# Optimization experiments

Measured on AMD Instinct MI355X. Metric: run time of the kernel, lower is better.

Reference implementation:

```python
import jax, jax.numpy as jnp
import numpy as np

L, N, D, R = 1024, 16384, 512, 128
PENALTY = -10000.0


def setup_inputs() -> dict:
    key = jax.random.key(0)
    k1, k2, k3, k4, k5 = jax.random.split(key, 5)
    unary_logits = jax.random.normal(k1, (L, N), jnp.float32)
    H = jax.random.normal(k2, (N, D), jnp.float32)
    limit = float(np.sqrt(6.0 / (D + D)))  # xavier_uniform for square W
    W = jax.random.uniform(k3, (D, D), jnp.float32, -limit, limit)
    gold = jax.random.randint(k4, (L,), 0, N)
    # dense reachability matrix: allowed[cur_label, prev_label]
    allowed = jax.random.bernoulli(k5, 0.05, (N, N))
    return {"unary_logits": unary_logits, "H": H, "W": W, "gold": gold,
            "allowed": allowed, "top_r": R}


def reference(unary_logits, H, W, gold, allowed, top_r):
    # --- candidate pruning: top_r distinct labels per step, sorted ---
    _, idx = jax.lax.top_k(unary_logits, top_r)      # [L, R]
    cand = jnp.sort(idx, axis=-1)                     # matches sorted(set(topi))

    # --- forward (alpha) recurrence over candidate sets ---
    alpha0 = jax.nn.log_softmax(jnp.take(unary_logits[0], cand[0]))

    def step(alpha, xs):
        prev, cur, u = xs                             # [R], [R], [N]
        pair = (H[prev] @ W) @ H[cur].T               # [R, R] bilinear
        mask = allowed[cur][:, prev].T                # mask[i, j] = prev_i reachable to cur_j
        pair = pair + jnp.where(mask, 0.0, PENALTY)
        new_alpha = (jax.scipy.special.logsumexp(alpha[:, None] + pair, axis=0)
                     + jax.nn.log_softmax(u[cur]))
        return new_alpha, None

    alpha_last, _ = jax.lax.scan(step, alpha0,
                                 (cand[:-1], cand[1:], unary_logits[1:]))
    logZ = jax.scipy.special.logsumexp(alpha_last)

    # --- gold path score ---
    t = jnp.arange(unary_logits.shape[0])
    score_unary = unary_logits[t, gold].sum()
    gp, gc = gold[:-1], gold[1:]
    trans = jnp.einsum('ld,de,le->l', H[gp], W, H[gc])
    score_pair = jnp.where(allowed[gc, gp], trans, PENALTY).sum()

    return logZ - (score_unary + score_pair)
```

## Files before the change

kernel.cpp:

```cpp
#include <hip/hip_runtime.h>

typedef unsigned short u16;
typedef __attribute__((ext_vector_type(8))) short s8v;
typedef __attribute__((ext_vector_type(8))) __bf16 bfv8;
typedef __attribute__((ext_vector_type(4))) float f32x4;

#define L_DIM 1024
#define N_DIM 16384
#define R_DIM 128
#define PEN  -10000.0f
#define MC_MIN 1e-35f

__device__ __forceinline__ float b2f(u16 x) { return __uint_as_float(((unsigned)x) << 16); }
__device__ __forceinline__ u16 f2bf(float f) {
    unsigned u = __float_as_uint(f);
    unsigned r = (u + 0x7FFFu + ((u >> 16) & 1u)) >> 16;
    return (u16)r;
}
__device__ __forceinline__ unsigned fmapu(float f) {
    unsigned u = __float_as_uint(f);
    return (u & 0x80000000u) ? ~u : (u | 0x80000000u);
}
__device__ __forceinline__ float funmap(unsigned u) {
    unsigned b = (u & 0x80000000u) ? (u & 0x7fffffffu) : ~u;
    return __uint_as_float(b);
}
__device__ __forceinline__ int mask_ok(const void* al, int fl, size_t idx) {
    if (fl) return ((const unsigned char*)al)[idx] != 0;
    return ((const unsigned*)al)[idx] != 0u;
}

__device__ __forceinline__ float blk_max(float x, float* scr) {
#pragma unroll
    for (int o = 32; o > 0; o >>= 1) x = fmaxf(x, __shfl_xor(x, o));
    __syncthreads();
    if ((threadIdx.x & 63) == 0) scr[threadIdx.x >> 6] = x;
    __syncthreads();
    return fmaxf(fmaxf(scr[0], scr[1]), fmaxf(scr[2], scr[3]));
}
__device__ __forceinline__ float blk_sum(float x, float* scr) {
#pragma unroll
    for (int o = 32; o > 0; o >>= 1) x += __shfl_xor(x, o);
    __syncthreads();
    if ((threadIdx.x & 63) == 0) scr[threadIdx.x >> 6] = x;
    __syncthreads();
    return scr[0] + scr[1] + scr[2] + scr[3];
}

__global__ void detect_k(const unsigned* __restrict__ a, int* __restrict__ flag) {
    int bad = 0;
    for (int i = threadIdx.x; i < 4096; i += 256) {
        unsigned w = a[i];
        if (w != 0u && w != 1u && w != 0x3F800000u) bad = 1;
    }
    if (bad) *flag = 1;
}

__global__ __launch_bounds__(256) void pack_mask_k(const void* __restrict__ al,
                                                   const int* __restrict__ flag,
                                                   unsigned* __restrict__ bits) {
    const size_t wi = (size_t)blockIdx.x * 256 + threadIdx.x;
    const int fl = *flag;
    unsigned out = 0u;
    if (fl) {
        const uint4* p = (const uint4*)((const unsigned char*)al + wi * 32);
        uint4 a = p[0], b = p[1];
        unsigned v[8] = {a.x, a.y, a.z, a.w, b.x, b.y, b.z, b.w};
#pragma unroll
        for (int q = 0; q < 8; ++q)
#pragma unroll
            for (int e = 0; e < 4; ++e)
                if ((v[q] >> (e * 8)) & 0xFFu) out |= 1u << (q * 4 + e);
    } else {
        const uint4* p = (const uint4*)((const unsigned*)al + wi * 32);
#pragma unroll
        for (int q = 0; q < 8; ++q) {
            uint4 a = p[q];
            if (a.x) out |= 1u << (q * 4 + 0);
            if (a.y) out |= 1u << (q * 4 + 1);
            if (a.z) out |= 1u << (q * 4 + 2);
            if (a.w) out |= 1u << (q * 4 + 3);
        }
    }
    bits[wi] = out;
}

__global__ __launch_bounds__(256) void topk_lsm_k(const float* __restrict__ U,
                                                  int* __restrict__ candg,
                                                  float* __restrict__ lsmg) {
    const int t = blockIdx.x;
    const float* row = U + (size_t)t * N_DIM;
    __shared__ unsigned hist[256];
    __shared__ int sel[2];
    __shared__ int cnts[2];
    __shared__ float vals[128];
    __shared__ int inds[128];
    __shared__ float scr[4];
    const int tid = threadIdx.x;
    unsigned prefix = 0;
    int kneed = 128;
    for (int pass = 0; pass < 4; ++pass) {
        const int sh = 24 - pass * 8;
        hist[tid] = 0;
        __syncthreads();
        for (int i = tid; i < N_DIM; i += 256) {
            unsigned u = __float_as_uint(row[i]);
            unsigned k = (u & 0x80000000u) ? ~u : (u | 0x80000000u);
            bool match = (pass == 0) || ((k >> (sh + 8)) == prefix);
            if (match) atomicAdd(&hist[(k >> sh) & 255u], 1u);
        }
        __syncthreads();
        if (tid == 0) {
            int acc = 0, d = 0;
            for (int dig = 255; dig >= 0; --dig) {
                int c = (int)hist[dig];
                if (acc + c >= kneed) { d = dig; break; }
                acc += c;
            }
            sel[0] = d; sel[1] = acc;
        }
        __syncthreads();
        kneed -= sel[1];
        prefix = (prefix << 8) | (unsigned)sel[0];
        __syncthreads();
    }
    const unsigned K = prefix;
    if (tid < 2) cnts[tid] = 0;
    if (tid < 128) { vals[tid] = -1.0e30f; inds[tid] = 0; }
    __syncthreads();
    for (int i = tid; i < N_DIM; i += 256) {
        float f = row[i];
        unsigned u = __float_as_uint(f);
        unsigned k = (u & 0x80000000u) ? ~u : (u | 0x80000000u);
        if (k > K) { int p = atomicAdd(&cnts[0], 1); if (p < 128) { vals[p] = f; inds[p] = i; } }
    }
    __syncthreads();
    const int cgt = min(cnts[0], 128);
    for (int i = tid; i < N_DIM; i += 256) {
        float f = row[i];
        unsigned u = __float_as_uint(f);
        unsigned k = (u & 0x80000000u) ? ~u : (u | 0x80000000u);
        if (k == K) {
            int p = atomicAdd(&cnts[1], 1);
            if (cgt + p < 128) { vals[cgt + p] = f; inds[cgt + p] = i; }
        }
    }
    __syncthreads();
    float xv = (tid < 128) ? vals[tid] : -3.0e38f;
    float mx = blk_max(xv, scr);
    float ex = (tid < 128) ? __expf(vals[tid] - mx) : 0.f;
    float sm = blk_sum(ex, scr);
    float lse = mx + __logf(fmaxf(sm, 1e-37f));
    if (tid < 128) {
        candg[t * 128 + tid] = min(max(inds[tid], 0), N_DIM - 1);
        lsmg[t * 128 + tid] = vals[tid] - lse;
    }
}

__global__ void cast_h_k(const float* __restrict__ H, u16* __restrict__ Hbf) {
    size_t base = ((size_t)blockIdx.x * 256 + threadIdx.x) * 4;
    float4 f = *(const float4*)(H + base);
    ushort4 o;
    o.x = f2bf(f.x); o.y = f2bf(f.y); o.z = f2bf(f.z); o.w = f2bf(f.w);
    *(ushort4*)(Hbf + base) = o;
}

__global__ __launch_bounds__(256) void gemm_hw_k(const float* __restrict__ H,
                                                 const float* __restrict__ W,
                                                 u16* __restrict__ HWbf) {
    const int r0 = blockIdx.x * 8;
    __shared__ float Hl[8][512];
    for (int idx = threadIdx.x; idx < 8 * 512; idx += 256) {
        int r = idx >> 9, k = idx & 511;
        Hl[r][k] = H[(size_t)(r0 + r) * 512 + k];
    }
    __syncthreads();
    const int c = threadIdx.x;
    float acc0[8], acc1[8];
#pragma unroll
    for (int r = 0; r < 8; ++r) { acc0[r] = 0.f; acc1[r] = 0.f; }
    for (int k = 0; k < 512; ++k) {
        float w0 = W[(size_t)k * 512 + c];
        float w1 = W[(size_t)k * 512 + c + 256];
#pragma unroll
        for (int r = 0; r < 8; ++r) {
            float h = Hl[r][k];
            acc0[r] += h * w0;
            acc1[r] += h * w1;
        }
    }
#pragma unroll
    for (int r = 0; r < 8; ++r) {
        HWbf[(size_t)(r0 + r) * 512 + c] = f2bf(acc0[r]);
        HWbf[(size_t)(r0 + r) * 512 + c + 256] = f2bf(acc1[r]);
    }
}

__global__ __launch_bounds__(256) void pair_k(const int* __restrict__ candg,
                                              const float* __restrict__ lsmg,
                                              const u16* __restrict__ HWbf,
                                              const u16* __restrict__ Hbf,
                                              const unsigned* __restrict__ bits,
                                              u16* __restrict__ Eg,
                                              float* __restrict__ cvec,
                                              float* __restrict__ gvec0) {
    const int t = blockIdx.x + 1;
    __shared__ __align__(16) u16 tile[2][128 * 64];
    __shared__ int sprev[128], scur[128];
    __shared__ unsigned maskw[128][4];
    __shared__ unsigned scm_u[128];
    __shared__ float cmf[128], cvf[128], wvv[128], scr[4];
    const int tid = threadIdx.x;
    if (tid < 128) {
        sprev[tid] = min(max(candg[(t - 1) * 128 + tid], 0), N_DIM - 1);
        scur[tid]  = min(max(candg[t * 128 + tid], 0), N_DIM - 1);
        scm_u[tid] = 0u;
    }
    __syncthreads();

    const int lane = tid & 63, w = tid >> 6;
    const int wr = w >> 1, wc = w & 1;
    const int srow = lane >> 3, slot = lane & 7;
    const int lq = lane & 15, lh = lane >> 4;

    const u16* pA[4]; const u16* pB[4]; int wadr[4];
#pragma unroll
    for (int q = 0; q < 4; ++q) {
        int r = (w * 4 + q) * 8 + srow;
        pA[q] = HWbf + (size_t)sprev[r] * 512 + slot * 8;
        pB[q] = Hbf  + (size_t)scur[r] * 512 + slot * 8;
        wadr[q] = r * 64 + ((slot ^ srow) * 8);
    }
    s8v rA[4], rB[4];
#pragma unroll
    for (int q = 0; q < 4; ++q) { rA[q] = *(const s8v*)pA[q]; rB[q] = *(const s8v*)pB[q]; }

    {
        const int j = tid & 127, ihalf = tid >> 7;
        const unsigned* rowp = bits + (size_t)scur[j] * 512;
        unsigned mw0 = 0u, mw1 = 0u;
#pragma unroll 8
        for (int kb = 0; kb < 32; ++kb) {
            int p0 = sprev[ihalf * 64 + kb];
            int p1 = sprev[ihalf * 64 + 32 + kb];
            mw0 |= ((rowp[p0 >> 5] >> (p0 & 31)) & 1u) << kb;
            mw1 |= ((rowp[p1 >> 5] >> (p1 & 31)) & 1u) << kb;
        }
        maskw[j][ihalf * 2]     = mw0;
        maskw[j][ihalf * 2 + 1] = mw1;
    }

    f32x4 acc[4][4];
#pragma unroll
    for (int a = 0; a < 4; ++a)
#pragma unroll
        for (int b = 0; b < 4; ++b) acc[a][b] = (f32x4){0.f, 0.f, 0.f, 0.f};

    for (int s = 0; s < 8; ++s) {
        __syncthreads();
#pragma unroll
        for (int q = 0; q < 4; ++q) {
            *(s8v*)&tile[0][wadr[q]] = rA[q];
            *(s8v*)&tile[1][wadr[q]] = rB[q];
        }
        __syncthreads();
        if (s < 7) {
#pragma unroll
            for (int q = 0; q < 4; ++q) {
                pA[q] += 64; pB[q] += 64;
                rA[q] = *(const s8v*)pA[q];
                rB[q] = *(const s8v*)pB[q];
            }
        }
#pragma unroll
        for (int kk = 0; kk < 2; ++kk) {
            bfv8 aF[4], bF[4];
            const int sl = (((kk << 2) | lh) ^ (lq & 7)) * 8;
#pragma unroll
            for (int b = 0; b < 4; ++b) {
                aF[b] = *(const bfv8*)&tile[0][(wr * 64 + b * 16 + lq) * 64 + sl];
                bF[b] = *(const bfv8*)&tile[1][(wc * 64 + b * 16 + lq) * 64 + sl];
            }
#pragma unroll
            for (int bi = 0; bi < 4; ++bi)
#pragma unroll
                for (int bj = 0; bj < 4; ++bj)
                    acc[bi][bj] = __builtin_amdgcn_mfma_f32_16x16x32_bf16(
                        aF[bi], bF[bj], acc[bi][bj], 0, 0, 0);
        }
    }

#pragma unroll
    for (int bj = 0; bj < 4; ++bj) {
        const int j = wc * 64 + bj * 16 + lq;
        float cm = -3.0e38f;
#pragma unroll
        for (int bi = 0; bi < 4; ++bi) {
#pragma unroll
            for (int r = 0; r < 4; ++r) {
                int i = wr * 64 + bi * 16 + lh * 4 + r;
                float v = acc[bi][bj][r];
                if (!((maskw[j][i >> 5] >> (i & 31)) & 1u)) v += PEN;
                acc[bi][bj][r] = v;
                cm = fmaxf(cm, v);
            }
        }
        cm = fmaxf(cm, __shfl_xor(cm, 16));
        cm = fmaxf(cm, __shfl_xor(cm, 32));
        if (lane < 16) atomicMax(&scm_u[j], fmapu(cm));
    }
    __syncthreads();
    if (tid < 128) {
        float cm = funmap(scm_u[tid]);
        cmf[tid] = cm;
        float cv = cm + lsmg[(size_t)t * 128 + tid];
        cvf[tid] = cv;
        cvec[(size_t)(t - 1) * 128 + tid] = cv;
    }
    __syncthreads();
    const int m = t - 1;
    const int roleA = ((m & 1) == 0) && (m != 1022);
    float xg = (tid < 128) ? cvf[tid] : -3.0e38f;
    float g = blk_max(xg, scr);
    if (tid == 0) gvec0[m] = g;
    if (tid < 128) wvv[tid] = roleA ? __expf(cvf[tid] - g) : 1.0f;
    __syncthreads();
    u16* Ebuf = &tile[0][0];
#pragma unroll
    for (int bj = 0; bj < 4; ++bj) {
        const int j = wc * 64 + bj * 16 + lq;
        const float cm = cmf[j];
        const float wj = wvv[j];
#pragma unroll
        for (int bi = 0; bi < 4; ++bi) {
#pragma unroll
            for (int r = 0; r < 4; ++r) {
                int i = wr * 64 + bi * 16 + lh * 4 + r;
                float e = __expf(acc[bi][bj][r] - cm);
                e = fminf(fmaxf(e, 0.f), 1.0f) * wj;
                Ebuf[i * 128 + j] = f2bf(e);
            }
        }
    }
    __syncthreads();
    u16* Eo = Eg + (size_t)(t - 1) * 16384;
    for (int idx = tid; idx < 2048; idx += 256)
        ((s8v*)Eo)[idx] = ((const s8v*)Ebuf)[idx];
}

__global__ __launch_bounds__(256) void score_k(const float* __restrict__ U,
                                               const int* __restrict__ gold,
                                               const void* __restrict__ allowed,
                                               const int* __restrict__ flag,
                                               const u16* __restrict__ HWbf,
                                               const u16* __restrict__ Hbf,
                                               float* __restrict__ accums) {
    const int t = blockIdx.x;
    __shared__ float scr[4];
    float part = 0.f;
    int gp = 0, gc = 0;
    if (t < L_DIM - 1) {
        gp = min(max(gold[t], 0), N_DIM - 1);
        gc = min(max(gold[t + 1], 0), N_DIM - 1);
        const u16* ar = HWbf + (size_t)gp * 512;
        const u16* br = Hbf + (size_t)gc * 512;
        for (int k = threadIdx.x; k < 512; k += 256)
            part += b2f(ar[k]) * b2f(br[k]);
    }
    float tot = blk_sum(part, scr);
    if (threadIdx.x == 0) {
        if (t < L_DIM - 1) {
            int ok = mask_ok(allowed, *flag, (size_t)gc * N_DIM + (size_t)gp);
            atomicAdd(&accums[1], ok ? tot : PEN);
        }
        int g0 = min(max(gold[t], 0), N_DIM - 1);
        atomicAdd(&accums[0], U[(size_t)t * N_DIM + g0]);
    }
}

__global__ __launch_bounds__(256) void mcomb_k(const u16* __restrict__ Gin,
                                               const float* __restrict__ cin,
                                               const float* __restrict__ gin,
                                               u16* __restrict__ Gout,
                                               float* __restrict__ cout,
                                               float* __restrict__ gout,
                                               int n_in, int last) {
    const int o = blockIdx.x;
    const int tid = threadIdx.x;
    __shared__ __align__(16) u16 As[128 * 136];
    __shared__ __align__(16) u16 BT[128 * 136];
    __shared__ float cb[128], rmc[128], wvv[128], scr[4];
    __shared__ unsigned scm[128];
    const u16* GA = Gin + (size_t)(2 * o) * 16384;
    u16* GO = Gout + (size_t)o * 16384;
    const int roleA = (!last) && ((o & 1) == 0);

    if (2 * o + 1 >= n_in) {
        if (tid < 128) {
            float cv = cin[(size_t)(2 * o) * 128 + tid];
            cb[tid] = cv;
            cout[(size_t)o * 128 + tid] = cv;
        }
        __syncthreads();
        float xg = (tid < 128) ? cb[tid] : -3.0e38f;
        float gp = blk_max(xg, scr);
        if (tid == 0 && gout) gout[o] = gp;
        if (tid < 128) {
            float d = cb[tid] - gp;
            wvv[tid] = roleA ? ((d > -80.f) ? __expf(d) : 0.f) : 1.0f;
        }
        __syncthreads();
        for (int idx = tid; idx < 2048; idx += 256) {
            s8v vv = ((const s8v*)GA)[idx];
            if (roleA) {
                const int j0 = (idx & 15) * 8;
#pragma unroll
                for (int e = 0; e < 8; ++e)
                    vv[e] = (short)f2bf(b2f((u16)vv[e]) * wvv[j0 + e]);
            }
            ((s8v*)GO)[idx] = vv;
        }
        return;
    }

    const float gA = gin[2 * o];
    const u16* GB = Gin + (size_t)(2 * o + 1) * 16384;
    if (tid < 128) {
        cb[tid] = cin[(size_t)(2 * o + 1) * 128 + tid];
        scm[tid] = 0u;
    }
    __syncthreads();
    if (tid < 128) {
        const s8v* src = (const s8v*)(GB + (size_t)tid * 128);
#pragma unroll
        for (int q = 0; q < 16; ++q) {
            s8v v = src[q];
#pragma unroll
            for (int e = 0; e < 8; ++e)
                BT[(q * 8 + e) * 136 + tid] = (u16)v[e];
        }
    } else {
        const int t0 = tid - 128;
#pragma unroll
        for (int q = 0; q < 16; ++q) {
            int gc = q * 128 + t0;
            int r = gc >> 4, qc = gc & 15;
            *(s8v*)&As[r * 136 + qc * 8] = *(const s8v*)(GA + (size_t)r * 128 + qc * 8);
        }
    }
    __syncthreads();

    const int lane = tid & 63, w = tid >> 6;
    const int wr = w >> 1, wc = w & 1;
    const int lq = lane & 15, lh = lane >> 4;
    f32x4 acc[4][4];
#pragma unroll
    for (int a = 0; a < 4; ++a)
#pragma unroll
        for (int b = 0; b < 4; ++b) acc[a][b] = (f32x4){0.f, 0.f, 0.f, 0.f};
#pragma unroll
    for (int kc = 0; kc < 4; ++kc) {
        bfv8 aF[4], bF[4];
        const int off = kc * 32 + lh * 8;
#pragma unroll
        for (int b = 0; b < 4; ++b) {
            aF[b] = *(const bfv8*)&As[(wr * 64 + b * 16 + lq) * 136 + off];
            bF[b] = *(const bfv8*)&BT[(wc * 64 + b * 16 + lq) * 136 + off];
        }
#pragma unroll
        for (int bi = 0; bi < 4; ++bi)
#pragma unroll
            for (int bj = 0; bj < 4; ++bj)
                acc[bi][bj] = __builtin_amdgcn_mfma_f32_16x16x32_bf16(
                    aF[bi], bF[bj], acc[bi][bj], 0, 0, 0);
    }
#pragma unroll
    for (int bj = 0; bj < 4; ++bj) {
        float cm = 0.f;
#pragma unroll
        for (int bi = 0; bi < 4; ++bi)
#pragma unroll
            for (int r = 0; r < 4; ++r) cm = fmaxf(cm, acc[bi][bj][r]);
        cm = fmaxf(cm, __shfl_xor(cm, 16));
        cm = fmaxf(cm, __shfl_xor(cm, 32));
        if (lane < 16) atomicMax(&scm[wc * 64 + bj * 16 + lq], __float_as_uint(cm));
    }
    __syncthreads();
    float cpv = -3.0e38f;
    if (tid < 128) {
        float mc = __uint_as_float(scm[tid]);
        if (mc > MC_MIN) {
            rmc[tid] = 1.0f / mc;
            cpv = cb[tid] + gA + __logf(mc);
            if (!(cpv > -1.0e29f)) cpv = -1.0e30f;
        } else {
            rmc[tid] = 0.f;
            cpv = -1.0e30f;
        }
        cout[(size_t)o * 128 + tid] = cpv;
    }
    float gp = blk_max(cpv, scr);
    if (tid == 0 && gout) gout[o] = gp;
    if (tid < 128) {
        float d = cpv - gp;
        wvv[tid] = roleA ? ((d > -80.f) ? __expf(d) : 0.f) : 1.0f;
    }
    __syncthreads();
#pragma unroll
    for (int bj = 0; bj < 4; ++bj) {
        const int k = wc * 64 + bj * 16 + lq;
        const float sc = rmc[k] * wvv[k];
#pragma unroll
        for (int bi = 0; bi < 4; ++bi)
#pragma unroll
            for (int r = 0; r < 4; ++r) {
                const int i = wr * 64 + bi * 16 + lh * 4 + r;
                float e = acc[bi][bj][r] * sc;
                e = fminf(fmaxf(e, 0.f), 1.0f);
                As[i * 136 + k] = f2bf(e);
            }
    }
    __syncthreads();
    for (int idx = tid; idx < 2048; idx += 256) {
        int r = idx >> 4, qc = idx & 15;
        *(s8v*)(GO + (size_t)r * 128 + qc * 8) = *(const s8v*)&As[r * 136 + qc * 8];
    }
}

__global__ __launch_bounds__(256) void tfinal2_k(const u16* __restrict__ G5,
                                                 const float* __restrict__ c5,
                                                 const float* __restrict__ lsmg,
                                                 const float* __restrict__ accums,
                                                 float* __restrict__ out) {
    __shared__ float v[128], ev[128], scr[4];
    __shared__ float psum[2][128];
    __shared__ __align__(16) u16 Gs[16384];
    const int tid = threadIdx.x;
    const int k = tid & 127, h = tid >> 7;
    if (tid < 128) v[tid] = lsmg[tid];
    __syncthreads();
    for (int s = 0; s < 32; ++s) {
        const u16* G = G5 + (size_t)s * 16384;
        for (int idx = tid; idx < 2048; idx += 256)
            ((s8v*)Gs)[idx] = ((const s8v*)G)[idx];
        float x = (tid < 128) ? v[tid] : -3.0e38f;
        float mv = blk_max(x, scr);
        if (tid < 128) {
            float d = v[tid] - mv;
            ev[tid] = (d > -80.f) ? __expf(d) : 0.f;
        }
        __syncthreads();
        float dot = 0.f;
        const int i0 = h * 64;
#pragma unroll 8
        for (int i = 0; i < 64; ++i)
            dot += ev[i0 + i] * b2f(Gs[(i0 + i) * 128 + k]);
        psum[h][k] = dot;
        __syncthreads();
        if (tid < 128) {
            float d = psum[0][tid] + psum[1][tid];
            v[tid] = (d > 0.f) ? (c5[s * 128 + tid] + mv + __logf(d)) : -1.0e30f;
        }
        __syncthreads();
    }
    float x = (tid < 128) ? v[tid] : -3.0e38f;
    float mz = blk_max(x, scr);
    float e = (tid < 128) ? __expf(v[tid] - mz) : 0.f;
    float sm = blk_sum(e, scr);
    if (tid == 0) out[0] = mz + __logf(fmaxf(sm, 1e-37f)) - (accums[0] + accums[1]);
}

extern "C" void kernel_launch(void* const* d_in, const int* in_sizes, int n_in,
                              void* d_out, int out_size, void* d_ws, size_t ws_size,
                              hipStream_t stream) {
    const float* U = (const float*)d_in[0];
    const float* H = (const float*)d_in[1];
    const float* W = (const float*)d_in[2];
    const int* gold = (const int*)d_in[3];
    const void* allowed = (const void*)d_in[4];

    char* ws = (char*)d_ws;
    float* accums = (float*)ws;
    int* flag = (int*)(ws + 8);
    size_t off = 256;
    int* cand = (int*)(ws + off);     off += (size_t)L_DIM * R_DIM * 4;
    float* lsm = (float*)(ws + off);  off += (size_t)L_DIM * R_DIM * 4;
    u16* Hbf = (u16*)(ws + off);      off += (size_t)N_DIM * 512 * 2;
    u16* HWbf = (u16*)(ws + off);     off += (size_t)N_DIM * 512 * 2;
    u16* E = (u16*)(ws + off);        off += (size_t)(L_DIM - 1) * 16384 * 2;
    float* cvec = (float*)(ws + off); off += (size_t)(L_DIM - 1) * 128 * 4;
    unsigned* bitsw = (unsigned*)(ws + off); off += (size_t)N_DIM * (N_DIM / 8);
    float* gvec0 = (float*)(ws + off); off += 1024 * 4;
    float* c1 = (float*)(ws + off); off += 512 * 128 * 4;
    float* g1 = (float*)(ws + off); off += 512 * 4;
    float* c2 = (float*)(ws + off); off += 256 * 128 * 4;
    float* g2 = (float*)(ws + off); off += 256 * 4;
    float* c3 = (float*)(ws + off); off += 128 * 128 * 4;
    float* g3 = (float*)(ws + off); off += 128 * 4;
    float* c4 = (float*)(ws + off); off += 64 * 128 * 4;
    float* g4 = (float*)(ws + off); off += 64 * 4;
    float* c5 = (float*)(ws + off); off += 32 * 128 * 4;

    u16* G1 = Hbf;
    u16* G2 = HWbf;
    u16* G3 = Hbf;
    u16* G4 = HWbf;
    u16* G5 = Hbf;

    hipMemsetAsync(d_ws, 0, 256, stream);
    detect_k<<<1, 256, 0, stream>>>((const unsigned*)d_in[4], flag);
    pack_mask_k<<<(int)(((size_t)N_DIM * N_DIM / 32) / 256), 256, 0, stream>>>(allowed, flag, bitsw);
    topk_lsm_k<<<L_DIM, 256, 0, stream>>>(U, cand, lsm);
    cast_h_k<<<(N_DIM * 512) / (256 * 4), 256, 0, stream>>>(H, Hbf);
    gemm_hw_k<<<N_DIM / 8, 256, 0, stream>>>(H, W, HWbf);
    pair_k<<<L_DIM - 1, 256, 0, stream>>>(cand, lsm, HWbf, Hbf, bitsw, E, cvec, gvec0);
    score_k<<<L_DIM, 256, 0, stream>>>(U, gold, allowed, flag, HWbf, Hbf, accums);
    mcomb_k<<<512, 256, 0, stream>>>(E, cvec, gvec0, G1, c1, g1, 1023, 0);
    mcomb_k<<<256, 256, 0, stream>>>(G1, c1, g1, G2, c2, g2, 512, 0);
    mcomb_k<<<128, 256, 0, stream>>>(G2, c2, g2, G3, c3, g3, 256, 0);
    mcomb_k<<<64, 256, 0, stream>>>(G3, c3, g3, G4, c4, g4, 128, 0);
    mcomb_k<<<32, 256, 0, stream>>>(G4, c4, g4, G5, c5, (float*)0, 64, 1);
    tfinal2_k<<<1, 256, 0, stream>>>(G5, c5, lsm, accums, (float*)d_out);
}
```

Measured before the change: 2.037 ms.

## Replace scalar H@W GEMM with bf16 MFMA tiled GEMM; per-wave top-k histograms

```diff
diff --git a/kernel.cpp b/kernel.cpp
--- a/kernel.cpp
+++ b/kernel.cpp
@@ -90,30 +90,33 @@
                                                   float* __restrict__ lsmg) {
     const int t = blockIdx.x;
     const float* row = U + (size_t)t * N_DIM;
-    __shared__ unsigned hist[256];
+    __shared__ unsigned hist[4][256];
     __shared__ int sel[2];
     __shared__ int cnts[2];
     __shared__ float vals[128];
     __shared__ int inds[128];
     __shared__ float scr[4];
     const int tid = threadIdx.x;
+    const int wv = tid >> 6;
     unsigned prefix = 0;
     int kneed = 128;
     for (int pass = 0; pass < 4; ++pass) {
         const int sh = 24 - pass * 8;
-        hist[tid] = 0;
+        for (int b = tid; b < 1024; b += 256) ((unsigned*)hist)[b] = 0;
         __syncthreads();
         for (int i = tid; i < N_DIM; i += 256) {
             unsigned u = __float_as_uint(row[i]);
             unsigned k = (u & 0x80000000u) ? ~u : (u | 0x80000000u);
             bool match = (pass == 0) || ((k >> (sh + 8)) == prefix);
-            if (match) atomicAdd(&hist[(k >> sh) & 255u], 1u);
-        }
+            if (match) atomicAdd(&hist[wv][(k >> sh) & 255u], 1u);
+        }
+        __syncthreads();
+        if (tid < 256) hist[0][tid] += hist[1][tid] + hist[2][tid] + hist[3][tid];
         __syncthreads();
         if (tid == 0) {
             int acc = 0, d = 0;
             for (int dig = 255; dig >= 0; --dig) {
-                int c = (int)hist[dig];
+                int c = (int)hist[0][dig];
                 if (acc + c >= kneed) { d = dig; break; }
                 acc += c;
             }
@@ -165,34 +168,86 @@
     *(ushort4*)(Hbf + base) = o;
 }
 
-__global__ __launch_bounds__(256) void gemm_hw_k(const float* __restrict__ H,
-                                                 const float* __restrict__ W,
-                                                 u16* __restrict__ HWbf) {
-    const int r0 = blockIdx.x * 8;
-    __shared__ float Hl[8][512];
-    for (int idx = threadIdx.x; idx < 8 * 512; idx += 256) {
-        int r = idx >> 9, k = idx & 511;
-        Hl[r][k] = H[(size_t)(r0 + r) * 512 + k];
-    }
-    __syncthreads();
-    const int c = threadIdx.x;
-    float acc0[8], acc1[8];
-#pragma unroll
-    for (int r = 0; r < 8; ++r) { acc0[r] = 0.f; acc1[r] = 0.f; }
-    for (int k = 0; k < 512; ++k) {
-        float w0 = W[(size_t)k * 512 + c];
-        float w1 = W[(size_t)k * 512 + c + 256];
-#pragma unroll
-        for (int r = 0; r < 8; ++r) {
-            float h = Hl[r][k];
-            acc0[r] += h * w0;
-            acc1[r] += h * w1;
-        }
-    }
-#pragma unroll
-    for (int r = 0; r < 8; ++r) {
-        HWbf[(size_t)(r0 + r) * 512 + c] = f2bf(acc0[r]);
-        HWbf[(size_t)(r0 + r) * 512 + c + 256] = f2bf(acc1[r]);
+__global__ __launch_bounds__(256) void cast_wT_k(const float* __restrict__ W,
+                                                 u16* __restrict__ WT) {
+    const int c = blockIdx.x;
+    for (int k = threadIdx.x; k < 512; k += 256)
+        WT[(size_t)c * 512 + k] = f2bf(W[(size_t)k * 512 + c]);
+}
+
+__global__ __launch_bounds__(256) void gemm_hw2_k(const u16* __restrict__ Hbf,
+                                                  const u16* __restrict__ WT,
+                                                  u16* __restrict__ HWbf) {
+    const int bm = blockIdx.x >> 2, bn = blockIdx.x & 3;
+    const int r0 = bm * 128, c0 = bn * 128;
+    __shared__ __align__(16) u16 tile[2][128 * 64];
+    const int tid = threadIdx.x;
+    const int lane = tid & 63, w = tid >> 6;
+    const int wr = w >> 1, wc = w & 1;
+    const int srow = lane >> 3, slot = lane & 7;
+    const int lq = lane & 15, lh = lane >> 4;
+
+    const u16* pA[4]; const u16* pB[4]; int wadr[4];
+#pragma unroll
+    for (int q = 0; q < 4; ++q) {
+        int r = (w * 4 + q) * 8 + srow;
+        pA[q] = Hbf + (size_t)(r0 + r) * 512 + slot * 8;
+        pB[q] = WT  + (size_t)(c0 + r) * 512 + slot * 8;
+        wadr[q] = r * 64 + ((slot ^ srow) * 8);
+    }
+    s8v rA[4], rB[4];
+#pragma unroll
+    for (int q = 0; q < 4; ++q) { rA[q] = *(const s8v*)pA[q]; rB[q] = *(const s8v*)pB[q]; }
+
+    f32x4 acc[4][4];
+#pragma unroll
+    for (int a = 0; a < 4; ++a)
+#pragma unroll
+        for (int b = 0; b < 4; ++b) acc[a][b] = (f32x4){0.f, 0.f, 0.f, 0.f};
+
+    for (int s = 0; s < 8; ++s) {
+        __syncthreads();
+#pragma unroll
+        for (int q = 0; q < 4; ++q) {
+            *(s8v*)&tile[0][wadr[q]] = rA[q];
+            *(s8v*)&tile[1][wadr[q]] = rB[q];
+        }
+        __syncthreads();
+        if (s < 7) {
+#pragma unroll
+            for (int q = 0; q < 4; ++q) {
+                pA[q] += 64; pB[q] += 64;
+                rA[q] = *(const s8v*)pA[q];
+                rB[q] = *(const s8v*)pB[q];
+            }
+        }
+#pragma unroll
+        for (int kk = 0; kk < 2; ++kk) {
+            bfv8 aF[4], bF[4];
+            const int sl = (((kk << 2) | lh) ^ (lq & 7)) * 8;
+#pragma unroll
+            for (int b = 0; b < 4; ++b) {
+                aF[b] = *(const bfv8*)&tile[0][(wr * 64 + b * 16 + lq) * 64 + sl];
+                bF[b] = *(const bfv8*)&tile[1][(wc * 64 + b * 16 + lq) * 64 + sl];
+            }
+#pragma unroll
+            for (int bi = 0; bi < 4; ++bi)
+#pragma unroll
+                for (int bj = 0; bj < 4; ++bj)
+                    acc[bi][bj] = __builtin_amdgcn_mfma_f32_16x16x32_bf16(
+                        aF[bi], bF[bj], acc[bi][bj], 0, 0, 0);
+        }
+    }
+#pragma unroll
+    for (int bj = 0; bj < 4; ++bj) {
+        const int j = wc * 64 + bj * 16 + lq;
+#pragma unroll
+        for (int bi = 0; bi < 4; ++bi)
+#pragma unroll
+            for (int r = 0; r < 4; ++r) {
+                const int i = wr * 64 + bi * 16 + lh * 4 + r;
+                HWbf[(size_t)(r0 + i) * 512 + c0 + j] = f2bf(acc[bi][bj][r]);
+            }
     }
 }
 
@@ -600,6 +655,7 @@
     float* c4 = (float*)(ws + off); off += 64 * 128 * 4;
     float* g4 = (float*)(ws + off); off += 64 * 4;
     float* c5 = (float*)(ws + off); off += 32 * 128 * 4;
+    u16* WbfT = (u16*)(ws + off);   off += (size_t)512 * 512 * 2;
 
     u16* G1 = Hbf;
     u16* G2 = HWbf;
@@ -612,7 +668,8 @@
     pack_mask_k<<<(int)(((size_t)N_DIM * N_DIM / 32) / 256), 256, 0, stream>>>(allowed, flag, bitsw);
     topk_lsm_k<<<L_DIM, 256, 0, stream>>>(U, cand, lsm);
     cast_h_k<<<(N_DIM * 512) / (256 * 4), 256, 0, stream>>>(H, Hbf);
-    gemm_hw_k<<<N_DIM / 8, 256, 0, stream>>>(H, W, HWbf);
+    cast_wT_k<<<512, 256, 0, stream>>>(W, WbfT);
+    gemm_hw2_k<<<512, 256, 0, stream>>>(Hbf, WbfT, HWbf);
     pair_k<<<L_DIM - 1, 256, 0, stream>>>(cand, lsm, HWbf, Hbf, bitsw, E, cvec, gvec0);
     score_k<<<L_DIM, 256, 0, stream>>>(U, gold, allowed, flag, HWbf, Hbf, accums);
     mcomb_k<<<512, 256, 0, stream>>>(E, cvec, gvec0, G1, c1, g1, 1023, 0);
```

Measured after the change: 1.918 ms. 5.8% less time.
